# Kernel tuning notes

Measured on AMD Instinct MI355X. Metric: run time of the kernel, lower is better.

## Reference

```python
import jax, jax.numpy as jnp
import numpy as np

DIM = 1024
NUM_EXPERTS = 8
TOP_K = 2
LOAD_BALANCE_WEIGHT = 0.01


def setup_inputs() -> dict:
    key = jax.random.key(0)
    ks = jax.random.split(key, 8)
    d, e, h = DIM, NUM_EXPERTS, 4 * DIM
    scale = 0.02
    return {
        "x": jax.random.normal(ks[0], (4, 2048, d), dtype=jnp.float32),
        "w_router": jax.random.normal(ks[1], (d, e), dtype=jnp.float32) * scale,
        "b_router": jnp.zeros((e,), dtype=jnp.float32),
        "w1": jax.random.normal(ks[2], (e, d, h), dtype=jnp.float32) * scale,
        "b1": jnp.zeros((e, h), dtype=jnp.float32),
        "w2": jax.random.normal(ks[3], (e, h, d), dtype=jnp.float32) * scale,
        "b2": jnp.zeros((e, d), dtype=jnp.float32),
    }


def reference(x, w_router, b_router, w1, b1, w2, b2):
    # x: [b, s, d]
    router_logits = jnp.einsum("bsd,de->bse", x, w_router) + b_router  # [b,s,E]
    probs = jax.nn.softmax(router_logits, axis=-1)
    routing_weights, selected_experts = jax.lax.top_k(probs, TOP_K)  # [b,s,K]
    routing_weights = routing_weights / routing_weights.sum(axis=-1, keepdims=True)

    output = jnp.zeros_like(x)
    for e in range(NUM_EXPERTS):
        # Dense per-expert MLP; tokens not routed to expert e get gate 0,
        # matching the masked scatter-add in the original module.
        h = jax.nn.gelu(jnp.einsum("bsd,dh->bsh", x, w1[e]) + b1[e], approximate=False)
        y = jnp.einsum("bsh,hd->bsd", h, w2[e]) + b2[e]
        gate = jnp.where(selected_experts == e, routing_weights, 0.0).sum(axis=-1)  # [b,s]
        output = output + y * gate[..., None]

    # Load-balance aux loss: var (unbiased, ddof=1) / mean of tokens-per-expert.
    one_hot = jax.nn.one_hot(selected_experts, NUM_EXPERTS, dtype=jnp.float32)  # [b,s,K,E]
    tokens_per_expert = one_hot.sum(axis=(0, 1, 2))  # [E]
    load_balance_loss = (jnp.var(tokens_per_expert, ddof=1) / tokens_per_expert.mean()) * LOAD_BALANCE_WEIGHT
    return output, load_balance_loss
```

## Files before the change

kernel.cpp:

```cpp
#include <hip/hip_runtime.h>
#include <math.h>

#define TOKENS 8192
#define DIM    1024
#define NEXP   8
#define HID    4096
#define TILE_M 128
#define MAX_TILES 136
#define BKS    32

#define BK     32
#define LDA    40
#define LDB    40

typedef __bf16 bf16x8 __attribute__((ext_vector_type(8)));
typedef float  f32x4  __attribute__((ext_vector_type(4)));
typedef unsigned int u32x4 __attribute__((ext_vector_type(4)));

__device__ __forceinline__ unsigned short f2bf(float f) {
  union { float f; unsigned u; } v; v.f = f;
  unsigned u = v.u + 0x7fffu + ((v.u >> 16) & 1u);
  return (unsigned short)(u >> 16);
}
__device__ __forceinline__ float gelu_f(float v) {
  return 0.5f * v * (1.f + erff(v * 0.7071067811865476f));
}
__device__ __forceinline__ float gelu_fast(float v) {
  float t = v * v;
  float y = 0.7978845608f * v * fmaf(t, 0.044715f, 1.0f);
  y = fminf(y, 15.f);
  float z = __expf(2.f * y);
  return v * z * __builtin_amdgcn_rcpf(1.f + z);
}
__device__ __forceinline__ void gload16(const void* g, void* l) {
  __builtin_amdgcn_global_load_lds(
      (const __attribute__((address_space(1))) void*)g,
      (__attribute__((address_space(3))) void*)l, 16, 0, 0);
}
__device__ __forceinline__ int xcd_swz(int id, int nwg) {
  int q = nwg >> 3, r = nwg & 7;
  int xcd = id & 7, rank = id >> 3;
  return (xcd < r) ? xcd * (q + 1) + rank : r * (q + 1) + (xcd - r) * q + rank;
}

__global__ __launch_bounds__(256) void k_router(
    const float* __restrict__ x, const float* __restrict__ wr,
    const float* __restrict__ br, int* __restrict__ sel,
    float* __restrict__ gates, int* __restrict__ counts,
    unsigned short* __restrict__ xb)
{
  int t = blockIdx.x * 4 + (threadIdx.x >> 6);
  int lane = threadIdx.x & 63;
  const float* xr = x + (size_t)t * DIM;
  unsigned short* xo = xb + (size_t)t * DIM;
  float acc[NEXP];
#pragma unroll
  for (int e = 0; e < NEXP; ++e) acc[e] = 0.f;
#pragma unroll
  for (int it = 0; it < 4; ++it) {
    int d = it * 256 + lane * 4;
    float4 xv = *(const float4*)(xr + d);
    ushort4 pk;
    pk.x = f2bf(xv.x); pk.y = f2bf(xv.y); pk.z = f2bf(xv.z); pk.w = f2bf(xv.w);
    *(ushort4*)(xo + d) = pk;
    float xs[4] = {xv.x, xv.y, xv.z, xv.w};
#pragma unroll
    for (int j = 0; j < 4; ++j) {
      float4 wa = *(const float4*)(wr + (size_t)(d + j) * NEXP);
      float4 wb = *(const float4*)(wr + (size_t)(d + j) * NEXP + 4);
      acc[0] += xs[j] * wa.x; acc[1] += xs[j] * wa.y;
      acc[2] += xs[j] * wa.z; acc[3] += xs[j] * wa.w;
      acc[4] += xs[j] * wb.x; acc[5] += xs[j] * wb.y;
      acc[6] += xs[j] * wb.z; acc[7] += xs[j] * wb.w;
    }
  }
#pragma unroll
  for (int off = 32; off >= 1; off >>= 1) {
#pragma unroll
    for (int e = 0; e < NEXP; ++e) acc[e] += __shfl_xor(acc[e], off);
  }
  if (lane == 0) {
    float l[NEXP];
#pragma unroll
    for (int e = 0; e < NEXP; ++e) l[e] = acc[e] + br[e];
    int e1 = 0; float v1 = l[0];
#pragma unroll
    for (int e = 1; e < NEXP; ++e) if (l[e] > v1) { v1 = l[e]; e1 = e; }
    int e2 = -1; float v2 = -1e30f;
#pragma unroll
    for (int e = 0; e < NEXP; ++e) {
      if (e == e1) continue;
      if (l[e] > v2) { v2 = l[e]; e2 = e; }
    }
    float g1 = 1.f / (1.f + expf(v2 - v1));
    sel[t * 2] = e1; sel[t * 2 + 1] = e2;
    gates[t * 2] = g1; gates[t * 2 + 1] = 1.f - g1;
    atomicAdd(&counts[e1], 1);
    atomicAdd(&counts[e2], 1);
  }
}

__global__ __launch_bounds__(256) void k_setup(
    const int* __restrict__ counts, int* __restrict__ cursors,
    int* __restrict__ ntiles_p, int* __restrict__ tile_expert,
    int* __restrict__ tile_row0, int* __restrict__ pair_token,
    float* __restrict__ pair_gate, float* __restrict__ loss_out)
{
  __shared__ int s_pad0[NEXP], s_pad1[NEXP];
  int tid = threadIdx.x;
  if (tid == 0) {
    int poff = 0, nt = 0;
    float var = 0.f;
    for (int e = 0; e < NEXP; ++e) {
      int c = counts[e];
      cursors[e] = poff;
      int ntl = (c + TILE_M - 1) / TILE_M;
      for (int i = 0; i < ntl; ++i) { tile_expert[nt] = e; tile_row0[nt] = poff + i * TILE_M; ++nt; }
      s_pad0[e] = poff + c;
      s_pad1[e] = poff + ntl * TILE_M;
      float d = (float)c - 2048.f;
      var += d * d;
      poff += ntl * TILE_M;
    }
    *ntiles_p = nt;
    *loss_out = (var * (1.f / 7.f)) * (1.f / 2048.f) * 0.01f;
  }
  __syncthreads();
#pragma unroll
  for (int e = 0; e < NEXP; ++e) {
    for (int r = s_pad0[e] + tid; r < s_pad1[e]; r += 256) {
      pair_token[r] = -1; pair_gate[r] = 0.f;
    }
  }
}

__global__ __launch_bounds__(256) void k_bucket(
    const int* __restrict__ sel, const float* __restrict__ gates,
    int* __restrict__ cursors, int* __restrict__ pair_token, float* __restrict__ pair_gate)
{
  int t = blockIdx.x * 256 + threadIdx.x;
#pragma unroll
  for (int k = 0; k < 2; ++k) {
    int e = sel[t * 2 + k];
    int pos = atomicAdd(&cursors[e], 1);
    pair_token[pos] = t;
    pair_gate[pos] = gates[t * 2 + k];
  }
}

__global__ __launch_bounds__(256) void k_castwT(
    const float* __restrict__ w, unsigned short* __restrict__ wT, int K, int N)
{
  __shared__ unsigned short t[64][72];
  int e = blockIdx.z, n0 = blockIdx.x * 64, k0 = blockIdx.y * 64;
  int tid = threadIdx.x;
  int kr = tid >> 2, nc = (tid & 3) * 16;
  const float* src = w + ((size_t)e * K + k0 + kr) * N + n0 + nc;
#pragma unroll
  for (int j = 0; j < 4; ++j) {
    f32x4 v = *(const f32x4*)(src + j * 4);
#pragma unroll
    for (int q = 0; q < 4; ++q) t[nc + j * 4 + q][kr] = f2bf(v[q]);
  }
  __syncthreads();
  int nr = tid >> 2, kc = (tid & 3) * 16;
  unsigned short* dst = wT + ((size_t)e * N + n0 + nr) * K + k0 + kc;
  *(u32x4*)dst = *(const u32x4*)&t[nr][kc];
  *(u32x4*)(dst + 8) = *(const u32x4*)&t[nr][kc + 8];
}

__global__ __launch_bounds__(256) void k_gemm1n(
    const unsigned short* __restrict__ xb, const unsigned short* __restrict__ w1T,
    const float* __restrict__ b1, const int* __restrict__ pair_token,
    const int* __restrict__ tile_expert, const int* __restrict__ tile_row0,
    const int* __restrict__ ntiles_p, unsigned short* __restrict__ h, int chunk_base)
{
  const int NBn = HID / 128;
  const int nwg = gridDim.x;
  int newid = xcd_swz(blockIdx.x, nwg);
  int ltile = newid / NBn, nb = newid - ltile * NBn;
  int tile = chunk_base + ltile;
  if (tile >= *ntiles_p) return;
  const int e = tile_expert[tile];
  const int row0 = tile_row0[tile];
  const int n0 = nb * 128;
  const int tid = threadIdx.x;
  const int w = tid >> 6, lane = tid & 63;

  __shared__ unsigned short As[2][128 * BKS];
  __shared__ unsigned short Bs[2][128 * BKS];
  __shared__ int tok[128];

  if (tid < 128) { int t = pair_token[row0 + tid]; tok[tid] = (t < 0) ? 0 : t; }
  __syncthreads();

  const int sr = lane >> 2;
  const int kq = (lane & 3) * 8;
  const int ar1 = w * 32 + sr, ar2 = ar1 + 16;
  const unsigned short* ag1 = xb + (size_t)tok[ar1] * DIM + kq;
  const unsigned short* ag2 = xb + (size_t)tok[ar2] * DIM + kq;
  const unsigned short* bg1 = w1T + ((size_t)e * HID + n0 + ar1) * DIM + kq;
  const unsigned short* bg2 = w1T + ((size_t)e * HID + n0 + ar2) * DIM + kq;

  const int wm = (w & 1) * 64, wn = (w >> 1) * 64;
  const int lr = lane & 15, lk = lane >> 4;

  f32x4 acc[4][4];
#pragma unroll
  for (int mi = 0; mi < 4; ++mi)
#pragma unroll
    for (int ni = 0; ni < 4; ++ni) acc[mi][ni] = {0.f, 0.f, 0.f, 0.f};

  {
    gload16(ag1, &As[0][(w * 32) * BKS]);
    gload16(ag2, &As[0][(w * 32 + 16) * BKS]);
    gload16(bg1, &Bs[0][(w * 32) * BKS]);
    gload16(bg2, &Bs[0][(w * 32 + 16) * BKS]);
  }
  asm volatile("s_waitcnt vmcnt(0)" ::: "memory");
  __builtin_amdgcn_s_barrier();

  const int NT = DIM / BKS;
  int cur = 0;
#pragma unroll 2
  for (int t = 0; t < NT; ++t) {
    int nxt = cur ^ 1;
    if (t + 1 < NT) {
      int k1 = (t + 1) * BKS;
      gload16(ag1 + k1, &As[nxt][(w * 32) * BKS]);
      gload16(ag2 + k1, &As[nxt][(w * 32 + 16) * BKS]);
      gload16(bg1 + k1, &Bs[nxt][(w * 32) * BKS]);
      gload16(bg2 + k1, &Bs[nxt][(w * 32 + 16) * BKS]);
    }
    bf16x8 af[4], bfr[4];
#pragma unroll
    for (int mi = 0; mi < 4; ++mi)
      af[mi] = *(const bf16x8*)&As[cur][(wm + mi * 16 + lr) * BKS + lk * 8];
#pragma unroll
    for (int ni = 0; ni < 4; ++ni)
      bfr[ni] = *(const bf16x8*)&Bs[cur][(wn + ni * 16 + lr) * BKS + lk * 8];
    asm volatile("s_waitcnt lgkmcnt(0)" ::: "memory");
    __builtin_amdgcn_sched_barrier(0);
    __builtin_amdgcn_s_setprio(1);
#pragma unroll
    for (int mi = 0; mi < 4; ++mi)
#pragma unroll
      for (int ni = 0; ni < 4; ++ni)
        acc[mi][ni] = __builtin_amdgcn_mfma_f32_16x16x32_bf16(bfr[ni], af[mi], acc[mi][ni], 0, 0, 0);
    __builtin_amdgcn_s_setprio(0);
    asm volatile("s_waitcnt vmcnt(0)" ::: "memory");
    __builtin_amdgcn_s_barrier();
    cur = nxt;
  }

  const size_t tl = (size_t)(tile - chunk_base);
  f32x4 bv[4];
#pragma unroll
  for (int ni = 0; ni < 4; ++ni)
    bv[ni] = *(const f32x4*)(b1 + (size_t)e * HID + n0 + wn + ni * 16 + lk * 4);
#pragma unroll
  for (int mi = 0; mi < 4; ++mi) {
    int m = wm + mi * 16 + lr;
    unsigned short* hrow = h + (tl * TILE_M + m) * HID + n0;
#pragma unroll
    for (int ni = 0; ni < 4; ++ni) {
      int nb4 = wn + ni * 16 + lk * 4;
      ushort4 pk;
      pk.x = f2bf(gelu_fast(acc[mi][ni][0] + bv[ni][0]));
      pk.y = f2bf(gelu_fast(acc[mi][ni][1] + bv[ni][1]));
      pk.z = f2bf(gelu_fast(acc[mi][ni][2] + bv[ni][2]));
      pk.w = f2bf(gelu_fast(acc[mi][ni][3] + bv[ni][3]));
      *(ushort4*)(hrow + nb4) = pk;
    }
  }
}

__global__ __launch_bounds__(256) void k_gemm2n(
    const unsigned short* __restrict__ h, const unsigned short* __restrict__ w2T,
    const float* __restrict__ b2, const int* __restrict__ pair_token,
    const float* __restrict__ pair_gate,
    const int* __restrict__ tile_expert, const int* __restrict__ tile_row0,
    const int* __restrict__ ntiles_p, float* __restrict__ out, int chunk_base)
{
  const int NBn = DIM / 128;
  const int nwg = gridDim.x;
  int newid = xcd_swz(blockIdx.x, nwg);
  int ltile = newid / NBn, nb = newid - ltile * NBn;
  int tile = chunk_base + ltile;
  if (tile >= *ntiles_p) return;
  const int e = tile_expert[tile];
  const int row0 = tile_row0[tile];
  const int n0 = nb * 128;
  const int tid = threadIdx.x;
  const int w = tid >> 6, lane = tid & 63;

  __shared__ unsigned short As[2][128 * BKS];
  __shared__ unsigned short Bs[2][128 * BKS];
  __shared__ int tok[128];
  __shared__ float gat[128];

  if (tid < 128) { tok[tid] = pair_token[row0 + tid]; gat[tid] = pair_gate[row0 + tid]; }
  __syncthreads();

  const int sr = lane >> 2;
  const int kq = (lane & 3) * 8;
  const int ar1 = w * 32 + sr, ar2 = ar1 + 16;
  const size_t tl = (size_t)(tile - chunk_base);
  const unsigned short* ag1 = h + (tl * TILE_M + ar1) * HID + kq;
  const unsigned short* ag2 = h + (tl * TILE_M + ar2) * HID + kq;
  const unsigned short* bg1 = w2T + ((size_t)e * DIM + n0 + ar1) * HID + kq;
  const unsigned short* bg2 = w2T + ((size_t)e * DIM + n0 + ar2) * HID + kq;

  const int wm = (w & 1) * 64, wn = (w >> 1) * 64;
  const int lr = lane & 15, lk = lane >> 4;

  f32x4 acc[4][4];
#pragma unroll
  for (int mi = 0; mi < 4; ++mi)
#pragma unroll
    for (int ni = 0; ni < 4; ++ni) acc[mi][ni] = {0.f, 0.f, 0.f, 0.f};

  {
    gload16(ag1, &As[0][(w * 32) * BKS]);
    gload16(ag2, &As[0][(w * 32 + 16) * BKS]);
    gload16(bg1, &Bs[0][(w * 32) * BKS]);
    gload16(bg2, &Bs[0][(w * 32 + 16) * BKS]);
  }
  asm volatile("s_waitcnt vmcnt(0)" ::: "memory");
  __builtin_amdgcn_s_barrier();

  const int NT = HID / BKS;
  int cur = 0;
#pragma unroll 2
  for (int t = 0; t < NT; ++t) {
    int nxt = cur ^ 1;
    if (t + 1 < NT) {
      int k1 = (t + 1) * BKS;
      gload16(ag1 + k1, &As[nxt][(w * 32) * BKS]);
      gload16(ag2 + k1, &As[nxt][(w * 32 + 16) * BKS]);
      gload16(bg1 + k1, &Bs[nxt][(w * 32) * BKS]);
      gload16(bg2 + k1, &Bs[nxt][(w * 32 + 16) * BKS]);
    }
    bf16x8 af[4], bfr[4];
#pragma unroll
    for (int mi = 0; mi < 4; ++mi)
      af[mi] = *(const bf16x8*)&As[cur][(wm + mi * 16 + lr) * BKS + lk * 8];
#pragma unroll
    for (int ni = 0; ni < 4; ++ni)
      bfr[ni] = *(const bf16x8*)&Bs[cur][(wn + ni * 16 + lr) * BKS + lk * 8];
    asm volatile("s_waitcnt lgkmcnt(0)" ::: "memory");
    __builtin_amdgcn_sched_barrier(0);
    __builtin_amdgcn_s_setprio(1);
#pragma unroll
    for (int mi = 0; mi < 4; ++mi)
#pragma unroll
      for (int ni = 0; ni < 4; ++ni)
        acc[mi][ni] = __builtin_amdgcn_mfma_f32_16x16x32_bf16(bfr[ni], af[mi], acc[mi][ni], 0, 0, 0);
    __builtin_amdgcn_s_setprio(0);
    asm volatile("s_waitcnt vmcnt(0)" ::: "memory");
    __builtin_amdgcn_s_barrier();
    cur = nxt;
  }

  f32x4 bv[4];
#pragma unroll
  for (int ni = 0; ni < 4; ++ni)
    bv[ni] = *(const f32x4*)(b2 + (size_t)e * DIM + n0 + wn + ni * 16 + lk * 4);
#pragma unroll
  for (int mi = 0; mi < 4; ++mi) {
    int m = wm + mi * 16 + lr;
    int t = tok[m];
    if (t >= 0) {
      float g = gat[m];
      float* orow = out + (size_t)t * DIM + n0;
#pragma unroll
      for (int ni = 0; ni < 4; ++ni) {
        int nb4 = wn + ni * 16 + lk * 4;
#pragma unroll
        for (int r = 0; r < 4; ++r)
          atomicAdd(orow + nb4 + r, (acc[mi][ni][r] + bv[ni][r]) * g);
      }
    }
  }
}

__global__ __launch_bounds__(256) void k_gemm1(
    const unsigned short* __restrict__ xb, const float* __restrict__ w1,
    const float* __restrict__ b1, const int* __restrict__ pair_token,
    const int* __restrict__ tile_expert, const int* __restrict__ tile_row0,
    const int* __restrict__ ntiles_p, unsigned short* __restrict__ h, int chunk_base)
{
  int tile = chunk_base + blockIdx.y;
  if (tile >= *ntiles_p) return;
  const int e = tile_expert[tile];
  const int row0 = tile_row0[tile];
  const int n0 = blockIdx.x * 128;
  const int tid = threadIdx.x;

  __shared__ unsigned short As[TILE_M * LDA];
  __shared__ unsigned short Bs[128 * LDB];
  __shared__ int tok[TILE_M];

  if (tid < TILE_M) tok[tid] = pair_token[row0 + tid];
  __syncthreads();

  const int ar = tid >> 1, akh = (tid & 1) * 16;
  const int bk = tid >> 3, bnh = (tid & 7) * 16;
  const int bswz = tid & 3;
  const int wv = tid >> 6, lane = tid & 63;
  const int wm = (wv & 1) * 64, wn = (wv >> 1) * 64;
  const int lr = lane & 15, lk = lane >> 4;
  const int atok = tok[ar];

  f32x4 acc[4][4];
#pragma unroll
  for (int mi = 0; mi < 4; ++mi)
#pragma unroll
    for (int ni = 0; ni < 4; ++ni) acc[mi][ni] = {0.f, 0.f, 0.f, 0.f};

  const unsigned short* asrc = (atok >= 0) ? (xb + (size_t)atok * DIM + akh) : (const unsigned short*)0;
  const float* bsrc0 = w1 + ((size_t)e * DIM + bk) * HID + n0 + bnh;
  const int wcol = 8 * ((bk >> 3) ^ bswz) + (bk & 7);

  for (int k0 = 0; k0 < DIM; k0 += BK) {
    u32x4 av0 = {0, 0, 0, 0}, av1 = {0, 0, 0, 0};
    if (asrc) {
      av0 = *(const u32x4*)(asrc + k0);
      av1 = *(const u32x4*)(asrc + k0 + 8);
    }
    float bv[16];
    const float* bs = bsrc0 + (size_t)k0 * HID;
#pragma unroll
    for (int j = 0; j < 4; ++j) {
      f32x4 f = *(const f32x4*)(bs + j * 4);
      bv[j * 4 + 0] = f[0]; bv[j * 4 + 1] = f[1];
      bv[j * 4 + 2] = f[2]; bv[j * 4 + 3] = f[3];
    }
    __syncthreads();
    *(u32x4*)&As[ar * LDA + akh] = av0;
    *(u32x4*)&As[ar * LDA + akh + 8] = av1;
#pragma unroll
    for (int j = 0; j < 16; ++j)
      Bs[(bnh + j) * LDB + wcol] = f2bf(bv[j]);
    __syncthreads();

    bf16x8 af[4], bfr[4];
#pragma unroll
    for (int mi = 0; mi < 4; ++mi)
      af[mi] = *(const bf16x8*)&As[(wm + mi * 16 + lr) * LDA + lk * 8];
#pragma unroll
    for (int ni = 0; ni < 4; ++ni) {
      int pch = lk ^ (((wn >> 4) + ni) & 3);
      bfr[ni] = *(const bf16x8*)&Bs[(wn + ni * 16 + lr) * LDB + pch * 8];
    }
#pragma unroll
    for (int mi = 0; mi < 4; ++mi)
#pragma unroll
      for (int ni = 0; ni < 4; ++ni)
        acc[mi][ni] = __builtin_amdgcn_mfma_f32_16x16x32_bf16(af[mi], bfr[ni], acc[mi][ni], 0, 0, 0);
  }

  const size_t tl = (size_t)(tile - chunk_base);
#pragma unroll
  for (int mi = 0; mi < 4; ++mi)
#pragma unroll
    for (int ni = 0; ni < 4; ++ni)
#pragma unroll
      for (int r = 0; r < 4; ++r) {
        int m = wm + mi * 16 + (lane >> 4) * 4 + r;
        int n = wn + ni * 16 + (lane & 15);
        float v = acc[mi][ni][r] + b1[(size_t)e * HID + n0 + n];
        h[(tl * TILE_M + m) * HID + n0 + n] = f2bf(gelu_f(v));
      }
}

__global__ __launch_bounds__(256) void k_gemm2(
    const unsigned short* __restrict__ h, const float* __restrict__ w2,
    const float* __restrict__ b2, const int* __restrict__ pair_token,
    const float* __restrict__ pair_gate,
    const int* __restrict__ tile_expert, const int* __restrict__ tile_row0,
    const int* __restrict__ ntiles_p, float* __restrict__ out, int chunk_base)
{
  int tile = chunk_base + blockIdx.y;
  if (tile >= *ntiles_p) return;
  const int e = tile_expert[tile];
  const int row0 = tile_row0[tile];
  const int n0 = blockIdx.x * 128;
  const int tid = threadIdx.x;

  __shared__ unsigned short As[TILE_M * LDA];
  __shared__ unsigned short Bs[128 * LDB];
  __shared__ int tok[TILE_M];
  __shared__ float gat[TILE_M];

  if (tid < TILE_M) { tok[tid] = pair_token[row0 + tid]; gat[tid] = pair_gate[row0 + tid]; }
  __syncthreads();

  const int ar = tid >> 1, akh = (tid & 1) * 16;
  const int bk = tid >> 3, bnh = (tid & 7) * 16;
  const int bswz = tid & 3;
  const int wv = tid >> 6, lane = tid & 63;
  const int wm = (wv & 1) * 64, wn = (wv >> 1) * 64;
  const int lr = lane & 15, lk = lane >> 4;

  f32x4 acc[4][4];
#pragma unroll
  for (int mi = 0; mi < 4; ++mi)
#pragma unroll
    for (int ni = 0; ni < 4; ++ni) acc[mi][ni] = {0.f, 0.f, 0.f, 0.f};

  const size_t tl = (size_t)(tile - chunk_base);
  const unsigned short* asrc = h + (tl * TILE_M + ar) * HID + akh;
  const float* bsrc0 = w2 + ((size_t)e * HID + bk) * DIM + n0 + bnh;
  const int wcol = 8 * ((bk >> 3) ^ bswz) + (bk & 7);

  for (int k0 = 0; k0 < HID; k0 += BK) {
    u32x4 av0 = *(const u32x4*)(asrc + k0);
    u32x4 av1 = *(const u32x4*)(asrc + k0 + 8);
    float bv[16];
    const float* bs = bsrc0 + (size_t)k0 * DIM;
#pragma unroll
    for (int j = 0; j < 4; ++j) {
      f32x4 f = *(const f32x4*)(bs + j * 4);
      bv[j * 4 + 0] = f[0]; bv[j * 4 + 1] = f[1];
      bv[j * 4 + 2] = f[2]; bv[j * 4 + 3] = f[3];
    }
    __syncthreads();
    *(u32x4*)&As[ar * LDA + akh] = av0;
    *(u32x4*)&As[ar * LDA + akh + 8] = av1;
#pragma unroll
    for (int j = 0; j < 16; ++j)
      Bs[(bnh + j) * LDB + wcol] = f2bf(bv[j]);
    __syncthreads();

    bf16x8 af[4], bfr[4];
#pragma unroll
    for (int mi = 0; mi < 4; ++mi)
      af[mi] = *(const bf16x8*)&As[(wm + mi * 16 + lr) * LDA + lk * 8];
#pragma unroll
    for (int ni = 0; ni < 4; ++ni) {
      int pch = lk ^ (((wn >> 4) + ni) & 3);
      bfr[ni] = *(const bf16x8*)&Bs[(wn + ni * 16 + lr) * LDB + pch * 8];
    }
#pragma unroll
    for (int mi = 0; mi < 4; ++mi)
#pragma unroll
      for (int ni = 0; ni < 4; ++ni)
        acc[mi][ni] = __builtin_amdgcn_mfma_f32_16x16x32_bf16(af[mi], bfr[ni], acc[mi][ni], 0, 0, 0);
  }

#pragma unroll
  for (int mi = 0; mi < 4; ++mi)
#pragma unroll
    for (int ni = 0; ni < 4; ++ni)
#pragma unroll
      for (int r = 0; r < 4; ++r) {
        int m = wm + mi * 16 + (lane >> 4) * 4 + r;
        int n = wn + ni * 16 + (lane & 15);
        int t = tok[m];
        if (t >= 0) {
          float v = acc[mi][ni][r] + b2[(size_t)e * DIM + n0 + n];
          atomicAdd(out + (size_t)t * DIM + n0 + n, v * gat[m]);
        }
      }
}

extern "C" void kernel_launch(void* const* d_in, const int* in_sizes, int n_in,
                              void* d_out, int out_size, void* d_ws, size_t ws_size,
                              hipStream_t stream) {
  const float* x  = (const float*)d_in[0];
  const float* wr = (const float*)d_in[1];
  const float* br = (const float*)d_in[2];
  const float* w1 = (const float*)d_in[3];
  const float* b1 = (const float*)d_in[4];
  const float* w2 = (const float*)d_in[5];
  const float* b2 = (const float*)d_in[6];
  float* out = (float*)d_out;

  char* ws = (char*)d_ws;
  int*   counts      = (int*)(ws + 0);
  int*   cursors     = (int*)(ws + 64);
  int*   ntiles      = (int*)(ws + 128);
  int*   tile_expert = (int*)(ws + 256);
  int*   tile_row0   = (int*)(ws + 1024);
  int*   sel         = (int*)(ws + 4096);
  float* gates       = (float*)(ws + 4096 + 65536);
  int*   pair_token  = (int*)(ws + 4096 + 131072);
  float* pair_gate   = (float*)(ws + 4096 + 131072 + 69632);

  const size_t OFF_XB  = 274432;
  const size_t XB_SZ   = (size_t)TOKENS * DIM * 2;
  const size_t OFF_W1T = OFF_XB + XB_SZ;
  const size_t WT_SZ   = (size_t)NEXP * DIM * HID * 2;
  const size_t OFF_W2T = OFF_W1T + WT_SZ;
  const size_t OFF_HN  = OFF_W2T + WT_SZ;
  const size_t tile_bytes = (size_t)TILE_M * HID * 2;

  unsigned short* xb  = (unsigned short*)(ws + OFF_XB);

  hipMemsetAsync(d_out, 0, (size_t)out_size * sizeof(float), stream);
  hipMemsetAsync(counts, 0, 64, stream);

  hipLaunchKernelGGL(k_router, dim3(TOKENS / 4), dim3(256), 0, stream,
                     x, wr, br, sel, gates, counts, xb);
  hipLaunchKernelGGL(k_setup, dim3(1), dim3(256), 0, stream,
                     counts, cursors, ntiles, tile_expert, tile_row0,
                     pair_token, pair_gate, out + (size_t)out_size - 1);
  hipLaunchKernelGGL(k_bucket, dim3(TOKENS / 256), dim3(256), 0, stream,
                     sel, gates, cursors, pair_token, pair_gate);

  bool newpath = ws_size >= OFF_HN + tile_bytes;

  if (newpath) {
    unsigned short* w1T = (unsigned short*)(ws + OFF_W1T);
    unsigned short* w2T = (unsigned short*)(ws + OFF_W2T);
    unsigned short* h   = (unsigned short*)(ws + OFF_HN);

    hipLaunchKernelGGL(k_castwT, dim3(HID / 64, DIM / 64, NEXP), dim3(256), 0, stream,
                       w1, w1T, DIM, HID);
    hipLaunchKernelGGL(k_castwT, dim3(DIM / 64, HID / 64, NEXP), dim3(256), 0, stream,
                       w2, w2T, HID, DIM);

    long long avail = (long long)ws_size - (long long)OFF_HN;
    int tpc = (int)(avail / (long long)tile_bytes);
    if (tpc < 1) tpc = 1;
    if (tpc > MAX_TILES) tpc = MAX_TILES;
    int nchunks = (MAX_TILES + tpc - 1) / tpc;

    for (int c = 0; c < nchunks; ++c) {
      hipLaunchKernelGGL(k_gemm1n, dim3(tpc * (HID / 128)), dim3(256), 0, stream,
                         xb, w1T, b1, pair_token, tile_expert, tile_row0, ntiles, h, c * tpc);
      hipLaunchKernelGGL(k_gemm2n, dim3(tpc * (DIM / 128)), dim3(256), 0, stream,
                         h, w2T, b2, pair_token, pair_gate, tile_expert, tile_row0, ntiles, out, c * tpc);
    }
  } else {
    unsigned short* h = (unsigned short*)(ws + OFF_W1T);
    long long avail = (long long)ws_size - (long long)OFF_W1T;
    int tpc = (avail > 0) ? (int)(avail / (long long)tile_bytes) : 0;
    if (tpc < 1) tpc = 1;
    if (tpc > MAX_TILES) tpc = MAX_TILES;
    int nchunks = (MAX_TILES + tpc - 1) / tpc;

    for (int c = 0; c < nchunks; ++c) {
      hipLaunchKernelGGL(k_gemm1, dim3(HID / 128, tpc), dim3(256), 0, stream,
                         xb, w1, b1, pair_token, tile_expert, tile_row0, ntiles, h, c * tpc);
      hipLaunchKernelGGL(k_gemm2, dim3(DIM / 128, tpc), dim3(256), 0, stream,
                         h, w2, b2, pair_token, pair_gate, tile_expert, tile_row0, ntiles, out, c * tpc);
    }
  }
}
```

Measured before the change: 956.9 us.

## Triple-buffer LDS in both expert GEMMs and transpose GEMM2 atomic epilogue

Both grouped expert GEMM kernels move from double to triple-buffered shared memory and prefetch two K-steps ahead. Each iteration now waits with vmcnt(4) instead of draining all global loads, so more load latency is hidden behind MFMA work. In GEMM2 the MFMA operand order is swapped so each lane holds four rows of one column, and the atomic epilogue is rewritten so that adjacent lanes hit adjacent output columns, which should coalesce the atomics better. This raises LDS use per block, which may lower occupancy, and the pipeline counting relies on exactly four outstanding loads per stage.

```diff
diff --git a/kernel.cpp b/kernel.cpp
--- a/kernel.cpp
+++ b/kernel.cpp
@@ -187,8 +187,8 @@
   const int tid = threadIdx.x;
   const int w = tid >> 6, lane = tid & 63;
 
-  __shared__ unsigned short As[2][128 * BKS];
-  __shared__ unsigned short Bs[2][128 * BKS];
+  __shared__ unsigned short As[3][128 * BKS];
+  __shared__ unsigned short Bs[3][128 * BKS];
   __shared__ int tok[128];
 
   if (tid < 128) { int t = pair_token[row0 + tid]; tok[tid] = (t < 0) ? 0 : t; }
@@ -211,27 +211,21 @@
 #pragma unroll
     for (int ni = 0; ni < 4; ++ni) acc[mi][ni] = {0.f, 0.f, 0.f, 0.f};
 
-  {
-    gload16(ag1, &As[0][(w * 32) * BKS]);
-    gload16(ag2, &As[0][(w * 32 + 16) * BKS]);
-    gload16(bg1, &Bs[0][(w * 32) * BKS]);
-    gload16(bg2, &Bs[0][(w * 32 + 16) * BKS]);
-  }
-  asm volatile("s_waitcnt vmcnt(0)" ::: "memory");
+#define STAGE1(buf, koff)                                      \
+  gload16(ag1 + (koff), &As[buf][(w * 32) * BKS]);             \
+  gload16(ag2 + (koff), &As[buf][(w * 32 + 16) * BKS]);        \
+  gload16(bg1 + (koff), &Bs[buf][(w * 32) * BKS]);             \
+  gload16(bg2 + (koff), &Bs[buf][(w * 32 + 16) * BKS]);
+
+  STAGE1(0, 0)
+  STAGE1(1, BKS)
+  asm volatile("s_waitcnt vmcnt(4)" ::: "memory");
   __builtin_amdgcn_s_barrier();
 
   const int NT = DIM / BKS;
-  int cur = 0;
-#pragma unroll 2
+  int cur = 0, dst = 2;
   for (int t = 0; t < NT; ++t) {
-    int nxt = cur ^ 1;
-    if (t + 1 < NT) {
-      int k1 = (t + 1) * BKS;
-      gload16(ag1 + k1, &As[nxt][(w * 32) * BKS]);
-      gload16(ag2 + k1, &As[nxt][(w * 32 + 16) * BKS]);
-      gload16(bg1 + k1, &Bs[nxt][(w * 32) * BKS]);
-      gload16(bg2 + k1, &Bs[nxt][(w * 32 + 16) * BKS]);
-    }
+    if (t + 2 < NT) { STAGE1(dst, (t + 2) * BKS) }
     bf16x8 af[4], bfr[4];
 #pragma unroll
     for (int mi = 0; mi < 4; ++mi)
@@ -248,10 +242,13 @@
       for (int ni = 0; ni < 4; ++ni)
         acc[mi][ni] = __builtin_amdgcn_mfma_f32_16x16x32_bf16(bfr[ni], af[mi], acc[mi][ni], 0, 0, 0);
     __builtin_amdgcn_s_setprio(0);
-    asm volatile("s_waitcnt vmcnt(0)" ::: "memory");
+    if (t + 2 < NT) { asm volatile("s_waitcnt vmcnt(4)" ::: "memory"); }
+    else            { asm volatile("s_waitcnt vmcnt(0)" ::: "memory"); }
     __builtin_amdgcn_s_barrier();
-    cur = nxt;
-  }
+    cur = (cur == 2) ? 0 : cur + 1;
+    dst = (dst == 2) ? 0 : dst + 1;
+  }
+#undef STAGE1
 
   const size_t tl = (size_t)(tile - chunk_base);
   f32x4 bv[4];
@@ -294,8 +291,8 @@
   const int tid = threadIdx.x;
   const int w = tid >> 6, lane = tid & 63;
 
-  __shared__ unsigned short As[2][128 * BKS];
-  __shared__ unsigned short Bs[2][128 * BKS];
+  __shared__ unsigned short As[3][128 * BKS];
+  __shared__ unsigned short Bs[3][128 * BKS];
   __shared__ int tok[128];
   __shared__ float gat[128];
 
@@ -320,27 +317,21 @@
 #pragma unroll
     for (int ni = 0; ni < 4; ++ni) acc[mi][ni] = {0.f, 0.f, 0.f, 0.f};
 
-  {
-    gload16(ag1, &As[0][(w * 32) * BKS]);
-    gload16(ag2, &As[0][(w * 32 + 16) * BKS]);
-    gload16(bg1, &Bs[0][(w * 32) * BKS]);
-    gload16(bg2, &Bs[0][(w * 32 + 16) * BKS]);
-  }
-  asm volatile("s_waitcnt vmcnt(0)" ::: "memory");
+#define STAGE2(buf, koff)                                      \
+  gload16(ag1 + (koff), &As[buf][(w * 32) * BKS]);             \
+  gload16(ag2 + (koff), &As[buf][(w * 32 + 16) * BKS]);        \
+  gload16(bg1 + (koff), &Bs[buf][(w * 32) * BKS]);             \
+  gload16(bg2 + (koff), &Bs[buf][(w * 32 + 16) * BKS]);
+
+  STAGE2(0, 0)
+  STAGE2(1, BKS)
+  asm volatile("s_waitcnt vmcnt(4)" ::: "memory");
   __builtin_amdgcn_s_barrier();
 
   const int NT = HID / BKS;
-  int cur = 0;
-#pragma unroll 2
+  int cur = 0, dst = 2;
   for (int t = 0; t < NT; ++t) {
-    int nxt = cur ^ 1;
-    if (t + 1 < NT) {
-      int k1 = (t + 1) * BKS;
-      gload16(ag1 + k1, &As[nxt][(w * 32) * BKS]);
-      gload16(ag2 + k1, &As[nxt][(w * 32 + 16) * BKS]);
-      gload16(bg1 + k1, &Bs[nxt][(w * 32) * BKS]);
-      gload16(bg2 + k1, &Bs[nxt][(w * 32 + 16) * BKS]);
-    }
+    if (t + 2 < NT) { STAGE2(dst, (t + 2) * BKS) }
     bf16x8 af[4], bfr[4];
 #pragma unroll
     for (int mi = 0; mi < 4; ++mi)
@@ -355,33 +346,34 @@
     for (int mi = 0; mi < 4; ++mi)
 #pragma unroll
       for (int ni = 0; ni < 4; ++ni)
-        acc[mi][ni] = __builtin_amdgcn_mfma_f32_16x16x32_bf16(bfr[ni], af[mi], acc[mi][ni], 0, 0, 0);
+        acc[mi][ni] = __builtin_amdgcn_mfma_f32_16x16x32_bf16(af[mi], bfr[ni], acc[mi][ni], 0, 0, 0);
     __builtin_amdgcn_s_setprio(0);
-    asm volatile("s_waitcnt vmcnt(0)" ::: "memory");
+    if (t + 2 < NT) { asm volatile("s_waitcnt vmcnt(4)" ::: "memory"); }
+    else            { asm volatile("s_waitcnt vmcnt(0)" ::: "memory"); }
     __builtin_amdgcn_s_barrier();
-    cur = nxt;
-  }
-
-  f32x4 bv[4];
-#pragma unroll
-  for (int ni = 0; ni < 4; ++ni)
-    bv[ni] = *(const f32x4*)(b2 + (size_t)e * DIM + n0 + wn + ni * 16 + lk * 4);
-#pragma unroll
-  for (int mi = 0; mi < 4; ++mi) {
-    int m = wm + mi * 16 + lr;
-    int t = tok[m];
-    if (t >= 0) {
-      float g = gat[m];
-      float* orow = out + (size_t)t * DIM + n0;
-#pragma unroll
-      for (int ni = 0; ni < 4; ++ni) {
-        int nb4 = wn + ni * 16 + lk * 4;
-#pragma unroll
-        for (int r = 0; r < 4; ++r)
-          atomicAdd(orow + nb4 + r, (acc[mi][ni][r] + bv[ni][r]) * g);
+    cur = (cur == 2) ? 0 : cur + 1;
+    dst = (dst == 2) ? 0 : dst + 1;
+  }
+#undef STAGE2
+
+  float bia[4];
+#pragma unroll
+  for (int ni = 0; ni < 4; ++ni) bia[ni] = b2[(size_t)e * DIM + n0 + wn + ni * 16 + lr];
+#pragma unroll
+  for (int mi = 0; mi < 4; ++mi)
+#pragma unroll
+    for (int r = 0; r < 4; ++r) {
+      int m = wm + mi * 16 + lk * 4 + r;
+      int t = tok[m];
+      if (t >= 0) {
+        float g = gat[m];
+#pragma unroll
+        for (int ni = 0; ni < 4; ++ni) {
+          int n = wn + ni * 16 + lr;
+          atomicAdd(out + (size_t)t * DIM + n0 + n, (acc[mi][ni][r] + bia[ni]) * g);
+        }
       }
     }
-  }
 }
 
 __global__ __launch_bounds__(256) void k_gemm1(
```

Result: faster. 827.8 us (-13.5%).
